# Kernel tuning notes

Hardware: AMD Instinct MI355X
Metric: run time of the kernel (lower is better)

## Reference

```python
import jax, jax.numpy as jnp
import numpy as np


def _bd(x, W, b):
    # block-diagonal linear: x [B, D] -> [B, Dout], W [H, D/H, Dout/H], b [Dout]
    B, D = x.shape
    H = W.shape[0]
    y = jnp.einsum('bhi,hio->bho', x.reshape(B, H, D // H), W)
    return y.reshape(B, -1) + b


def setup_inputs() -> dict:
    key = jax.random.key(0)
    ks = jax.random.split(key, 16)
    B, D, H = 8192, 1024, 8
    U = int(D * 4 / 3)  # 1365
    d = D // H          # 128
    s = 0.05
    f32 = jnp.float32
    return {
        'x': jax.random.normal(ks[0], (B, D), f32),
        'h_prev': jax.random.normal(ks[1], (B, D), f32),
        'c_prev': jax.random.normal(ks[2], (B, D), f32),
        'n_prev': jax.random.uniform(ks[3], (B, D), f32) + 0.5,  # positive normalizer state
        'm_prev': jax.random.normal(ks[4], (B, D), f32),
        'ln_g': jnp.ones((D,), f32),
        'ln_b': jnp.zeros((D,), f32),
        'conv_w': jax.random.normal(ks[5], (1, 1, 4), f32) * 0.5,
        'conv_b': jax.random.normal(ks[6], (1,), f32) * 0.1,
        'W': jax.random.normal(ks[7], (4, H, d, d), f32) * s,   # gates z,i,f,o input projections
        'bW': jax.random.normal(ks[8], (4, D), f32) * s,
        'R': jax.random.normal(ks[9], (4, H, d, d), f32) * s,   # gates z,i,f,o recurrent projections
        'bR': jax.random.normal(ks[10], (4, D), f32) * s,
        'upl_w': jax.random.normal(ks[11], (D, U), f32) * s,
        'upl_b': jnp.zeros((U,), f32),
        'upr_w': jax.random.normal(ks[12], (D, U), f32) * s,
        'upr_b': jnp.zeros((U,), f32),
        'down_w': jax.random.normal(ks[13], (U, D), f32) * s,
        'down_b': jnp.zeros((D,), f32),
    }


def reference(x, h_prev, c_prev, n_prev, m_prev, ln_g, ln_b, conv_w, conv_b,
              W, bW, R, bR, upl_w, upl_b, upr_w, upr_b, down_w, down_b):
    # LayerNorm over feature dim (eps matches torch default 1e-5)
    mu = jnp.mean(x, axis=-1, keepdims=True)
    var = jnp.var(x, axis=-1, keepdims=True)
    x_norm = (x - mu) * jax.lax.rsqrt(var + 1e-5) * ln_g + ln_b
    # causal conv1d along the feature axis: kernel 4, left-pad 3 (Conv1d(1,1,4))
    conv = jax.lax.conv_general_dilated(
        x_norm[:, None, :], conv_w, window_strides=(1,), padding=[(3, 0)],
        dimension_numbers=('NCH', 'OIH', 'NCH'))[:, 0, :] + conv_b
    x_conv = jax.nn.silu(conv)
    # block-diagonal gate pre-activations (gate order in W/R stacks: z, i, f, o)
    z = jnp.tanh(_bd(x, W[0], bW[0]) + _bd(h_prev, R[0], bR[0]))
    o = jax.nn.sigmoid(_bd(x, W[3], bW[3]) + _bd(h_prev, R[3], bR[3]))
    i_tilde = _bd(x_conv, W[1], bW[1]) + _bd(h_prev, R[1], bR[1])
    f_tilde = _bd(x_conv, W[2], bW[2]) + _bd(h_prev, R[2], bR[2])
    # stabilized exp-max gating
    m_t = jnp.maximum(f_tilde + m_prev, i_tilde)
    i = jnp.exp(i_tilde - m_t)
    f = jnp.exp(f_tilde + m_prev - m_t)
    c_t = f * c_prev + i * z
    n_t = f * n_prev + i
    h_t = o * c_t / n_t
    # gated MLP (torch F.gelu default = exact erf gelu)
    left = h_t @ upl_w + upl_b
    right = jax.nn.gelu(h_t @ upr_w + upr_b, approximate=False)
    output = (left * right) @ down_w + down_b
    return (output, h_t, c_t, n_t, m_t)
```

## Files before the change

### kernel.cpp

```cpp
#include <hip/hip_runtime.h>
#include <hip/hip_bf16.h>

typedef __attribute__((ext_vector_type(8))) short s8v;
typedef __attribute__((ext_vector_type(4))) float f4v;
typedef unsigned short us4 __attribute__((ext_vector_type(4)));

#define NB 8192
#define ND 1024
#define NH 8
#define NU 1365
#define NUP 1408
#define GK 384
#define GN 512
static const size_t BD = (size_t)NB * ND;

#define WS_AG   ((size_t)0)
#define WS_PRE  ((size_t)0)
#define WS_G    ((size_t)50331648)
#define WS_HBF  ((size_t)73400320)
#define WS_WG   ((size_t)90177536)
#define WS_UPLT ((size_t)93323264)
#define WS_UPRT ((size_t)96206848)
#define WS_DWNT ((size_t)99090432)

__device__ __forceinline__ void gload16(const void* g, void* l) {
  __builtin_amdgcn_global_load_lds((const __attribute__((address_space(1))) void*)g,
                                   (__attribute__((address_space(3))) void*)l, 16, 0, 0);
}
__device__ __forceinline__ unsigned short tobf(float f) {
  unsigned int u = __float_as_uint(f);
  unsigned int r = (u + 0x7FFFu + ((u >> 16) & 1u)) >> 16;
  return (unsigned short)r;
}
__device__ __forceinline__ float frombf(unsigned short u) {
  return __uint_as_float(((unsigned int)u) << 16);
}
__device__ __forceinline__ float sigm(float x) { return 1.f / (1.f + expf(-x)); }
__device__ __forceinline__ f4v mfma16(s8v a, s8v b, f4v c) {
  return __builtin_amdgcn_mfma_f32_16x16x32_bf16(a, b, c, 0, 0, 0);
}

__global__ __launch_bounds__(256) void prep_kernel(
    const float* __restrict__ W, const float* __restrict__ R,
    const float* __restrict__ upl, const float* __restrict__ upr,
    const float* __restrict__ dwn,
    unsigned short* __restrict__ Wg, unsigned short* __restrict__ Lt,
    unsigned short* __restrict__ Rt, unsigned short* __restrict__ Dt) {
  long long idx = (long long)blockIdx.x * 256 + threadIdx.x;
  const long long N1 = (long long)NH * GN * GK;
  const long long N2 = (long long)NUP * ND;
  if (idx < N1) {
    int h = (int)(idx / (GN * GK));
    int rem = (int)(idx % (GN * GK));
    int n = rem / GK, kk = rem % GK;
    int g = n >> 7, j = n & 127;
    float v = 0.f;
    if (kk < 128) {
      if (g == 0 || g == 3) v = W[(((size_t)g * NH + h) * 128 + kk) * 128 + j];
    } else if (kk < 256) {
      if (g == 1 || g == 2) v = W[(((size_t)g * NH + h) * 128 + (kk - 128)) * 128 + j];
    } else {
      v = R[(((size_t)g * NH + h) * 128 + (kk - 256)) * 128 + j];
    }
    Wg[idx] = tobf(v);
    return;
  }
  idx -= N1;
  if (idx < N2) { int n = (int)(idx / ND), k = (int)(idx % ND);
    Lt[idx] = (n < NU) ? tobf(upl[(size_t)k * NU + n]) : 0; return; }
  idx -= N2;
  if (idx < N2) { int n = (int)(idx / ND), k = (int)(idx % ND);
    Rt[idx] = (n < NU) ? tobf(upr[(size_t)k * NU + n]) : 0; return; }
  idx -= N2;
  if (idx < N2) { int n = (int)(idx / NUP), k = (int)(idx % NUP);
    Dt[idx] = (k < NU) ? tobf(dwn[(size_t)k * ND + n]) : 0; return; }
}

__global__ __launch_bounds__(256) void norm_conv(
    const float* __restrict__ x, const float* __restrict__ hp,
    const float* __restrict__ lg, const float* __restrict__ lb,
    const float* __restrict__ cw, const float* __restrict__ cb,
    unsigned short* __restrict__ Ag) {
  const int b = blockIdx.x, tid = threadIdx.x;
  const int lane = tid & 63, wv = tid >> 6;
  __shared__ float xs[1024];
  __shared__ float red[8];
  const int d0 = tid * 4;
  float4 xv = *(const float4*)(x + (size_t)b * ND + d0);
  float s = xv.x + xv.y + xv.z + xv.w;
  float ss = xv.x * xv.x + xv.y * xv.y + xv.z * xv.z + xv.w * xv.w;
#pragma unroll
  for (int o = 32; o; o >>= 1) { s += __shfl_down(s, o); ss += __shfl_down(ss, o); }
  if (lane == 0) { red[wv] = s; red[4 + wv] = ss; }
  __syncthreads();
  float S = red[0] + red[1] + red[2] + red[3];
  float SS = red[4] + red[5] + red[6] + red[7];
  float mu = S * (1.f / ND);
  float var = SS * (1.f / ND) - mu * mu;
  float rstd = rsqrtf(var + 1e-5f);
  float xn[4];
#pragma unroll
  for (int t = 0; t < 4; ++t) {
    float xx = (&xv.x)[t];
    xn[t] = (xx - mu) * rstd * lg[d0 + t] + lb[d0 + t];
    xs[d0 + t] = xn[t];
  }
  __syncthreads();
  float w0 = cw[0], w1 = cw[1], w2 = cw[2], w3 = cw[3], cbv = cb[0];
  float cv[4];
#pragma unroll
  for (int t = 0; t < 4; ++t) {
    int d = d0 + t;
    float a = cbv + w3 * xs[d];
    if (d >= 1) a += w2 * xs[d - 1];
    if (d >= 2) a += w1 * xs[d - 2];
    if (d >= 3) a += w0 * xs[d - 3];
    cv[t] = a * (1.f / (1.f + expf(-a)));
  }
  float4 hv = *(const float4*)(hp + (size_t)b * ND + d0);
  const int h = d0 >> 7, j = d0 & 127;
  us4 px, pc, ph;
#pragma unroll
  for (int t = 0; t < 4; ++t) { px[t] = tobf((&xv.x)[t]); pc[t] = tobf(cv[t]); ph[t] = tobf((&hv.x)[t]); }
  size_t base = (size_t)b * 3072 + (size_t)h * 384 + j;
  *(us4*)(Ag + base) = px;
  *(us4*)(Ag + base + 128) = pc;
  *(us4*)(Ag + base + 256) = ph;
}

__global__ __launch_bounds__(256) void gate_fused(
    const unsigned short* __restrict__ Ag, const unsigned short* __restrict__ Wg,
    const float* __restrict__ bW, const float* __restrict__ bR,
    const float* __restrict__ cp, const float* __restrict__ np_,
    const float* __restrict__ mp,
    float* __restrict__ dout, unsigned short* __restrict__ Hb) {
  __shared__ short As[64 * 32];
  __shared__ short Bs[4][64 * 32];
  __shared__ float epi[4][16 * 68];
  const int tid = threadIdx.x, lane = tid & 63, wv = tid >> 6;
  const int row0 = blockIdx.x * 64, n0 = blockIdx.y, h = blockIdx.z;
  const int lr = lane >> 2, lc = (lane & 3) * 8;
  f4v acc[4][4] = {};
  const unsigned short* Bbase = Wg + ((size_t)h * GN + (size_t)wv * 128 + n0 * 64) * GK;
  for (int kt = 0; kt < GK / 32; ++kt) {
    const int k0 = kt * 32;
    gload16(Ag + (size_t)(row0 + wv * 16 + lr) * 3072 + (size_t)h * 384 + k0 + lc,
            (char*)As + wv * 1024);
#pragma unroll
    for (int q = 0; q < 4; ++q)
      gload16(Bbase + (size_t)(q * 16 + lr) * GK + k0 + lc,
              (char*)Bs[wv] + q * 1024);
    __syncthreads();
    s8v a[4], b[4];
#pragma unroll
    for (int m = 0; m < 4; ++m) a[m] = *(const s8v*)&As[(m * 16 + (lane & 15)) * 32 + (lane >> 4) * 8];
#pragma unroll
    for (int n = 0; n < 4; ++n) b[n] = *(const s8v*)&Bs[wv][(n * 16 + (lane & 15)) * 32 + (lane >> 4) * 8];
#pragma unroll
    for (int m = 0; m < 4; ++m)
#pragma unroll
      for (int n = 0; n < 4; ++n) acc[m][n] = mfma16(a[m], b[n], acc[m][n]);
    __syncthreads();
  }
  const int rr = tid >> 4;
  const int cc = (tid & 15) * 4;
  const int gcol = h * 128 + n0 * 64 + cc;
  float4 bz = *(const float4*)(bW + 0 * ND + gcol);
  float4 bi = *(const float4*)(bW + 1 * ND + gcol);
  float4 bf = *(const float4*)(bW + 2 * ND + gcol);
  float4 bo = *(const float4*)(bW + 3 * ND + gcol);
  float4 rz = *(const float4*)(bR + 0 * ND + gcol);
  float4 ri = *(const float4*)(bR + 1 * ND + gcol);
  float4 rf = *(const float4*)(bR + 2 * ND + gcol);
  float4 ro = *(const float4*)(bR + 3 * ND + gcol);
  bz.x += rz.x; bz.y += rz.y; bz.z += rz.z; bz.w += rz.w;
  bi.x += ri.x; bi.y += ri.y; bi.z += ri.z; bi.w += ri.w;
  bf.x += rf.x; bf.y += rf.y; bf.z += rf.z; bf.w += rf.w;
  bo.x += ro.x; bo.y += ro.y; bo.z += ro.z; bo.w += ro.w;
#pragma unroll
  for (int m = 0; m < 4; ++m) {
#pragma unroll
    for (int n = 0; n < 4; ++n)
#pragma unroll
      for (int r = 0; r < 4; ++r)
        epi[wv][((lane >> 4) * 4 + r) * 68 + n * 16 + (lane & 15)] = acc[m][n][r];
    __syncthreads();
    float4 zp = *(const float4*)&epi[0][rr * 68 + cc];
    float4 ip = *(const float4*)&epi[1][rr * 68 + cc];
    float4 fp = *(const float4*)&epi[2][rr * 68 + cc];
    float4 op = *(const float4*)&epi[3][rr * 68 + cc];
    const size_t grow = (size_t)(row0 + m * 16 + rr);
    const size_t base = grow * ND + gcol;
    float4 cv = *(const float4*)(cp + base);
    float4 nv = *(const float4*)(np_ + base);
    float4 mv = *(const float4*)(mp + base);
    float4 ho, co, no, mo;
    us4 hb;
#define GATE(c, k, BZ, BI, BF, BO)                          \
  { float zt = tanhf(zp.c + BZ); float ot = sigm(op.c + BO);\
    float it = ip.c + BI; float ft = fp.c + BF;             \
    float mt = fmaxf(ft + mv.c, it);                        \
    float ii = expf(it - mt);                               \
    float ff = expf(ft + mv.c - mt);                        \
    float ct = ff * cv.c + ii * zt;                         \
    float nt = ff * nv.c + ii;                              \
    float ht = ot * ct / nt;                                \
    ho.c = ht; co.c = ct; no.c = nt; mo.c = mt; hb[k] = tobf(ht); }
    GATE(x, 0, bz.x, bi.x, bf.x, bo.x)
    GATE(y, 1, bz.y, bi.y, bf.y, bo.y)
    GATE(z, 2, bz.z, bi.z, bf.z, bo.z)
    GATE(w, 3, bz.w, bi.w, bf.w, bo.w)
#undef GATE
    *(float4*)(dout + 1 * BD + base) = ho;
    *(float4*)(dout + 2 * BD + base) = co;
    *(float4*)(dout + 3 * BD + base) = no;
    *(float4*)(dout + 4 * BD + base) = mo;
    *(us4*)(Hb + base) = hb;
    __syncthreads();
  }
}

__global__ __launch_bounds__(256) void up_gemm(
    const unsigned short* __restrict__ A, const unsigned short* __restrict__ BL,
    const unsigned short* __restrict__ BR, unsigned short* __restrict__ Pre) {
  __shared__ short As[4096];
  __shared__ short Bs[4096];
  const int tid = threadIdx.x, lane = tid & 63, wv = tid >> 6;
  const int wm = wv >> 1, wn = wv & 1;
  const int row0 = blockIdx.x * 128, n0 = blockIdx.y * 128, zi = blockIdx.z;
  const unsigned short* Bt = zi ? BR : BL;
  unsigned short* O = Pre + (size_t)zi * NB * NUP;
  const int srow = wv * 32 + (lane >> 2), scol = (lane & 3) * 8;
  f4v acc[4][4] = {};
  for (int kt = 0; kt < 32; ++kt) {
    const int k0 = kt * 32;
    gload16(A + (size_t)(row0 + srow) * 1024 + k0 + scol, (char*)As + wv * 2048);
    gload16(A + (size_t)(row0 + srow + 16) * 1024 + k0 + scol, (char*)As + wv * 2048 + 1024);
    gload16(Bt + (size_t)(n0 + srow) * 1024 + k0 + scol, (char*)Bs + wv * 2048);
    gload16(Bt + (size_t)(n0 + srow + 16) * 1024 + k0 + scol, (char*)Bs + wv * 2048 + 1024);
    __syncthreads();
    s8v a[4], b[4];
#pragma unroll
    for (int m = 0; m < 4; ++m) a[m] = *(const s8v*)&As[(wm * 64 + m * 16 + (lane & 15)) * 32 + (lane >> 4) * 8];
#pragma unroll
    for (int n = 0; n < 4; ++n) b[n] = *(const s8v*)&Bs[(wn * 64 + n * 16 + (lane & 15)) * 32 + (lane >> 4) * 8];
#pragma unroll
    for (int m = 0; m < 4; ++m)
#pragma unroll
      for (int n = 0; n < 4; ++n) acc[m][n] = mfma16(a[m], b[n], acc[m][n]);
    __syncthreads();
  }
#pragma unroll
  for (int m = 0; m < 4; ++m) {
    const int row = row0 + wm * 64 + m * 16 + (lane >> 4) * 4;
#pragma unroll
    for (int n = 0; n < 4; ++n) {
      const int col = n0 + wn * 64 + n * 16 + (lane & 15);
#pragma unroll
      for (int r = 0; r < 4; ++r)
        O[(size_t)(row + r) * NUP + col] = tobf(acc[m][n][r]);
    }
  }
}

__global__ __launch_bounds__(256) void glu_elem(
    const unsigned short* __restrict__ Pre, const float* __restrict__ lbias,
    const float* __restrict__ rbias, unsigned short* __restrict__ G) {
  size_t i4 = (size_t)blockIdx.x * 256 + threadIdx.x;
  int col4 = (int)(i4 % 352);
  size_t row = i4 / 352;
  size_t base = row * NUP + (size_t)col4 * 4;
  us4 lv = *(const us4*)(Pre + base);
  us4 rv = *(const us4*)(Pre + (size_t)NB * NUP + base);
  us4 g;
#pragma unroll
  for (int t = 0; t < 4; ++t) {
    int col = col4 * 4 + t;
    if (col < NU) {
      float L = frombf(lv[t]) + lbias[col];
      float Rv = frombf(rv[t]) + rbias[col];
      float ge = 0.5f * Rv * (1.f + erff(Rv * 0.70710678118654752f));
      g[t] = tobf(L * ge);
    } else g[t] = 0;
  }
  *(us4*)(G + base) = g;
}

__global__ __launch_bounds__(256) void down_gemm(
    const unsigned short* __restrict__ A, const unsigned short* __restrict__ Bt,
    const float* __restrict__ dbias, float* __restrict__ out) {
  __shared__ short As[4096];
  __shared__ short Bs[4096];
  const int tid = threadIdx.x, lane = tid & 63, wv = tid >> 6;
  const int wm = wv >> 1, wn = wv & 1;
  const int row0 = blockIdx.x * 128, n0 = blockIdx.y * 128;
  const int srow = wv * 32 + (lane >> 2), scol = (lane & 3) * 8;
  f4v acc[4][4] = {};
  for (int kt = 0; kt < NUP / 32; ++kt) {
    const int k0 = kt * 32;
    gload16(A + (size_t)(row0 + srow) * NUP + k0 + scol, (char*)As + wv * 2048);
    gload16(A + (size_t)(row0 + srow + 16) * NUP + k0 + scol, (char*)As + wv * 2048 + 1024);
    gload16(Bt + (size_t)(n0 + srow) * NUP + k0 + scol, (char*)Bs + wv * 2048);
    gload16(Bt + (size_t)(n0 + srow + 16) * NUP + k0 + scol, (char*)Bs + wv * 2048 + 1024);
    __syncthreads();
    s8v a[4], b[4];
#pragma unroll
    for (int m = 0; m < 4; ++m) a[m] = *(const s8v*)&As[(wm * 64 + m * 16 + (lane & 15)) * 32 + (lane >> 4) * 8];
#pragma unroll
    for (int n = 0; n < 4; ++n) b[n] = *(const s8v*)&Bs[(wn * 64 + n * 16 + (lane & 15)) * 32 + (lane >> 4) * 8];
#pragma unroll
    for (int m = 0; m < 4; ++m)
#pragma unroll
      for (int n = 0; n < 4; ++n) acc[m][n] = mfma16(a[m], b[n], acc[m][n]);
    __syncthreads();
  }
#pragma unroll
  for (int m = 0; m < 4; ++m) {
    const int row = row0 + wm * 64 + m * 16 + (lane >> 4) * 4;
#pragma unroll
    for (int n = 0; n < 4; ++n) {
      const int col = n0 + wn * 64 + n * 16 + (lane & 15);
      const float bias = dbias[col];
#pragma unroll
      for (int r = 0; r < 4; ++r)
        out[(size_t)(row + r) * ND + col] = acc[m][n][r] + bias;
    }
  }
}

extern "C" void kernel_launch(void* const* d_in, const int* in_sizes, int n_in,
                              void* d_out, int out_size, void* d_ws, size_t ws_size,
                              hipStream_t stream) {
  const float* x    = (const float*)d_in[0];
  const float* hp   = (const float*)d_in[1];
  const float* cp   = (const float*)d_in[2];
  const float* np_  = (const float*)d_in[3];
  const float* mp   = (const float*)d_in[4];
  const float* lg   = (const float*)d_in[5];
  const float* lb   = (const float*)d_in[6];
  const float* cw   = (const float*)d_in[7];
  const float* cb   = (const float*)d_in[8];
  const float* W    = (const float*)d_in[9];
  const float* bW   = (const float*)d_in[10];
  const float* R    = (const float*)d_in[11];
  const float* bR   = (const float*)d_in[12];
  const float* upl  = (const float*)d_in[13];
  const float* uplb = (const float*)d_in[14];
  const float* upr  = (const float*)d_in[15];
  const float* uprb = (const float*)d_in[16];
  const float* dwn  = (const float*)d_in[17];
  const float* dwnb = (const float*)d_in[18];
  float* out = (float*)d_out;
  char* ws = (char*)d_ws;
  unsigned short* Ag  = (unsigned short*)(ws + WS_AG);
  unsigned short* Pre = (unsigned short*)(ws + WS_PRE);
  unsigned short* G   = (unsigned short*)(ws + WS_G);
  unsigned short* Hb  = (unsigned short*)(ws + WS_HBF);
  unsigned short* Wg  = (unsigned short*)(ws + WS_WG);
  unsigned short* Lt  = (unsigned short*)(ws + WS_UPLT);
  unsigned short* Rt  = (unsigned short*)(ws + WS_UPRT);
  unsigned short* Dt  = (unsigned short*)(ws + WS_DWNT);

  prep_kernel<<<23040, 256, 0, stream>>>(W, R, upl, upr, dwn, Wg, Lt, Rt, Dt);
  norm_conv<<<NB, 256, 0, stream>>>(x, hp, lg, lb, cw, cb, Ag);
  gate_fused<<<dim3(128, 2, 8), 256, 0, stream>>>(Ag, Wg, bW, bR, cp, np_, mp, out, Hb);
  up_gemm<<<dim3(64, 11, 2), 256, 0, stream>>>(Hb, Lt, Rt, Pre);
  glu_elem<<<11264, 256, 0, stream>>>(Pre, uplb, uprb, G);
  down_gemm<<<dim3(64, 8), 256, 0, stream>>>(G, Dt, dwnb, out);
}
```

Measured before the change: 282.0 us.

## Fuse GLU epilogue into up-projection GEMM with interleaved left/right weights

The left and right up-projection weights are interleaved in 16-column groups so a single GEMM tile computes matching left and right outputs. The bias, exact-erf GELU and product are then applied in the epilogue. This removes the separate bf16 pre-activation buffers (two 8192x1408 tensors), their write and re-read, and one kernel launch. Both GEMMs also switch to a 1D grid with a swizzled block order to improve L2 reuse of weight tiles, at the cost of more register pressure in the epilogue.

```diff
diff --git a/kernel.cpp b/kernel.cpp
--- a/kernel.cpp
+++ b/kernel.cpp
@@ -15,12 +15,10 @@
 static const size_t BD = (size_t)NB * ND;
 
 #define WS_AG   ((size_t)0)
-#define WS_PRE  ((size_t)0)
 #define WS_G    ((size_t)50331648)
 #define WS_HBF  ((size_t)73400320)
 #define WS_WG   ((size_t)90177536)
-#define WS_UPLT ((size_t)93323264)
-#define WS_UPRT ((size_t)96206848)
+#define WS_ULR  ((size_t)93323264)
 #define WS_DWNT ((size_t)99090432)
 
 __device__ __forceinline__ void gload16(const void* g, void* l) {
@@ -44,10 +42,11 @@
     const float* __restrict__ W, const float* __restrict__ R,
     const float* __restrict__ upl, const float* __restrict__ upr,
     const float* __restrict__ dwn,
-    unsigned short* __restrict__ Wg, unsigned short* __restrict__ Lt,
-    unsigned short* __restrict__ Rt, unsigned short* __restrict__ Dt) {
+    unsigned short* __restrict__ Wg, unsigned short* __restrict__ ULR,
+    unsigned short* __restrict__ Dt) {
   long long idx = (long long)blockIdx.x * 256 + threadIdx.x;
   const long long N1 = (long long)NH * GN * GK;
+  const long long N3 = (long long)2 * NUP * ND;
   const long long N2 = (long long)NUP * ND;
   if (idx < N1) {
     int h = (int)(idx / (GN * GK));
@@ -66,12 +65,16 @@
     return;
   }
   idx -= N1;
-  if (idx < N2) { int n = (int)(idx / ND), k = (int)(idx % ND);
-    Lt[idx] = (n < NU) ? tobf(upl[(size_t)k * NU + n]) : 0; return; }
-  idx -= N2;
-  if (idx < N2) { int n = (int)(idx / ND), k = (int)(idx % ND);
-    Rt[idx] = (n < NU) ? tobf(upr[(size_t)k * NU + n]) : 0; return; }
-  idx -= N2;
+  if (idx < N3) {
+    int r = (int)(idx / ND), k = (int)(idx % ND);
+    int o = (r >> 4) & 1;
+    int gcol = (r >> 5) * 16 + (r & 15);
+    float v = 0.f;
+    if (gcol < NU) v = o ? upr[(size_t)k * NU + gcol] : upl[(size_t)k * NU + gcol];
+    ULR[idx] = tobf(v);
+    return;
+  }
+  idx -= N3;
   if (idx < N2) { int n = (int)(idx / NUP), k = (int)(idx % NUP);
     Dt[idx] = (k < NU) ? tobf(dwn[(size_t)k * ND + n]) : 0; return; }
 }
@@ -221,23 +224,24 @@
 }
 
 __global__ __launch_bounds__(256) void up_gemm(
-    const unsigned short* __restrict__ A, const unsigned short* __restrict__ BL,
-    const unsigned short* __restrict__ BR, unsigned short* __restrict__ Pre) {
+    const unsigned short* __restrict__ A, const unsigned short* __restrict__ ULR,
+    const float* __restrict__ lbias, const float* __restrict__ rbias,
+    unsigned short* __restrict__ G) {
   __shared__ short As[4096];
   __shared__ short Bs[4096];
   const int tid = threadIdx.x, lane = tid & 63, wv = tid >> 6;
   const int wm = wv >> 1, wn = wv & 1;
-  const int row0 = blockIdx.x * 128, n0 = blockIdx.y * 128, zi = blockIdx.z;
-  const unsigned short* Bt = zi ? BR : BL;
-  unsigned short* O = Pre + (size_t)zi * NB * NUP;
+  const int bid = blockIdx.x;
+  const int swz = (bid & 7) * 176 + (bid >> 3);
+  const int row0 = (swz / 22) * 128, n0 = (swz % 22) * 128;
   const int srow = wv * 32 + (lane >> 2), scol = (lane & 3) * 8;
   f4v acc[4][4] = {};
   for (int kt = 0; kt < 32; ++kt) {
     const int k0 = kt * 32;
     gload16(A + (size_t)(row0 + srow) * 1024 + k0 + scol, (char*)As + wv * 2048);
     gload16(A + (size_t)(row0 + srow + 16) * 1024 + k0 + scol, (char*)As + wv * 2048 + 1024);
-    gload16(Bt + (size_t)(n0 + srow) * 1024 + k0 + scol, (char*)Bs + wv * 2048);
-    gload16(Bt + (size_t)(n0 + srow + 16) * 1024 + k0 + scol, (char*)Bs + wv * 2048 + 1024);
+    gload16(ULR + (size_t)(n0 + srow) * 1024 + k0 + scol, (char*)Bs + wv * 2048);
+    gload16(ULR + (size_t)(n0 + srow + 16) * 1024 + k0 + scol, (char*)Bs + wv * 2048 + 1024);
     __syncthreads();
     s8v a[4], b[4];
 #pragma unroll
@@ -250,40 +254,25 @@
       for (int n = 0; n < 4; ++n) acc[m][n] = mfma16(a[m], b[n], acc[m][n]);
     __syncthreads();
   }
+  const int gb = (n0 >> 1) + wn * 32;
 #pragma unroll
   for (int m = 0; m < 4; ++m) {
     const int row = row0 + wm * 64 + m * 16 + (lane >> 4) * 4;
 #pragma unroll
-    for (int n = 0; n < 4; ++n) {
-      const int col = n0 + wn * 64 + n * 16 + (lane & 15);
-#pragma unroll
-      for (int r = 0; r < 4; ++r)
-        O[(size_t)(row + r) * NUP + col] = tobf(acc[m][n][r]);
+    for (int p = 0; p < 2; ++p) {
+      const int gcol = gb + p * 16 + (lane & 15);
+      const bool ok = gcol < NU;
+      const float bl_ = ok ? lbias[gcol] : 0.f;
+      const float br_ = ok ? rbias[gcol] : 0.f;
+#pragma unroll
+      for (int r = 0; r < 4; ++r) {
+        float L = acc[m][2 * p][r] + bl_;
+        float Rv = acc[m][2 * p + 1][r] + br_;
+        float ge = 0.5f * Rv * (1.f + erff(Rv * 0.70710678118654752f));
+        G[(size_t)(row + r) * NUP + gcol] = ok ? tobf(L * ge) : (unsigned short)0;
+      }
     }
   }
-}
-
-__global__ __launch_bounds__(256) void glu_elem(
-    const unsigned short* __restrict__ Pre, const float* __restrict__ lbias,
-    const float* __restrict__ rbias, unsigned short* __restrict__ G) {
-  size_t i4 = (size_t)blockIdx.x * 256 + threadIdx.x;
-  int col4 = (int)(i4 % 352);
-  size_t row = i4 / 352;
-  size_t base = row * NUP + (size_t)col4 * 4;
-  us4 lv = *(const us4*)(Pre + base);
-  us4 rv = *(const us4*)(Pre + (size_t)NB * NUP + base);
-  us4 g;
-#pragma unroll
-  for (int t = 0; t < 4; ++t) {
-    int col = col4 * 4 + t;
-    if (col < NU) {
-      float L = frombf(lv[t]) + lbias[col];
-      float Rv = frombf(rv[t]) + rbias[col];
-      float ge = 0.5f * Rv * (1.f + erff(Rv * 0.70710678118654752f));
-      g[t] = tobf(L * ge);
-    } else g[t] = 0;
-  }
-  *(us4*)(G + base) = g;
 }
 
 __global__ __launch_bounds__(256) void down_gemm(
@@ -293,7 +282,9 @@
   __shared__ short Bs[4096];
   const int tid = threadIdx.x, lane = tid & 63, wv = tid >> 6;
   const int wm = wv >> 1, wn = wv & 1;
-  const int row0 = blockIdx.x * 128, n0 = blockIdx.y * 128;
+  const int bid = blockIdx.x;
+  const int swz = (bid & 7) * 64 + (bid >> 3);
+  const int row0 = (swz >> 3) * 128, n0 = (swz & 7) * 128;
   const int srow = wv * 32 + (lane >> 2), scol = (lane & 3) * 8;
   f4v acc[4][4] = {};
   for (int kt = 0; kt < NUP / 32; ++kt) {
@@ -353,18 +344,15 @@
   float* out = (float*)d_out;
   char* ws = (char*)d_ws;
   unsigned short* Ag  = (unsigned short*)(ws + WS_AG);
-  unsigned short* Pre = (unsigned short*)(ws + WS_PRE);
   unsigned short* G   = (unsigned short*)(ws + WS_G);
   unsigned short* Hb  = (unsigned short*)(ws + WS_HBF);
   unsigned short* Wg  = (unsigned short*)(ws + WS_WG);
-  unsigned short* Lt  = (unsigned short*)(ws + WS_UPLT);
-  unsigned short* Rt  = (unsigned short*)(ws + WS_UPRT);
+  unsigned short* ULR = (unsigned short*)(ws + WS_ULR);
   unsigned short* Dt  = (unsigned short*)(ws + WS_DWNT);
 
-  prep_kernel<<<23040, 256, 0, stream>>>(W, R, upl, upr, dwn, Wg, Lt, Rt, Dt);
+  prep_kernel<<<23040, 256, 0, stream>>>(W, R, upl, upr, dwn, Wg, ULR, Dt);
   norm_conv<<<NB, 256, 0, stream>>>(x, hp, lg, lb, cw, cb, Ag);
   gate_fused<<<dim3(128, 2, 8), 256, 0, stream>>>(Ag, Wg, bW, bR, cp, np_, mp, out, Hb);
-  up_gemm<<<dim3(64, 11, 2), 256, 0, stream>>>(Hb, Lt, Rt, Pre);
-  glu_elem<<<11264, 256, 0, stream>>>(Pre, uplb, uprb, G);
-  down_gemm<<<dim3(64, 8), 256, 0, stream>>>(G, Dt, dwnb, out);
-}
+  up_gemm<<<1408, 256, 0, stream>>>(Hb, ULR, uplb, uprb, G);
+  down_gemm<<<512, 256, 0, stream>>>(G, Dt, dwnb, out);
+}
```

Result: faster. 252.8 us (-10.4%).
